# Performance work log

Measured on AMD Instinct MI355X. Metric: run time of the kernel, lower is better.

The kernel has to match this reference:

```python
import jax, jax.numpy as jnp
import numpy as np

B, N, D, H = 8, 2048, 768, 12
HD = D // H
SCALE = HD ** -0.5


def setup_inputs() -> dict:
    key = jax.random.key(0)
    ks = jax.random.split(key, 5)
    std = D ** -0.5
    return {
        "x": jax.random.normal(ks[0], (B, N, D), jnp.float32),
        "W_qkv": jax.random.normal(ks[1], (D, 3 * D), jnp.float32) * std,
        "b_qkv": jax.random.normal(ks[2], (3 * D,), jnp.float32) * 0.02,
        "W_out": jax.random.normal(ks[3], (D, D), jnp.float32) * std,
        "b_out": jax.random.normal(ks[4], (D,), jnp.float32) * 0.02,
    }


def reference(x, W_qkv, b_qkv, W_out, b_out):
    qkv = x @ W_qkv + b_qkv
    qkv = qkv.reshape(B, N, 3, H, HD).transpose(2, 0, 3, 1, 4)
    q, k, v = qkv[0], qkv[1], qkv[2]
    # scaled dot-product attention (dropout is identity in eval)
    attn = jnp.einsum("bhqd,bhkd->bhqk", q, k) * SCALE
    attn = jax.nn.softmax(attn, axis=-1)
    out = jnp.einsum("bhqk,bhkd->bhqd", attn, v)
    out = out.transpose(0, 2, 1, 3).reshape(B, N, D)
    return out @ W_out + b_out
```

## Files before the change

### kernel.cpp

```cpp
#include <hip/hip_runtime.h>
#include <hip/hip_bf16.h>
#include <stdint.h>

#define BB 8
#define NN 2048
#define DD 768
#define HH 12
#define HD 64
#define ND3 2304
#define TOK (BB*NN)
#define QSC 0.18033688011112042f

typedef __bf16 bf16x8 __attribute__((ext_vector_type(8)));
typedef float  f32x4  __attribute__((ext_vector_type(4)));
typedef float  f32x16 __attribute__((ext_vector_type(16)));
typedef unsigned uint2v __attribute__((ext_vector_type(2)));

__device__ __forceinline__ unsigned short f2bf(float f) {
    union { float f; unsigned u; } v; v.f = f;
    unsigned r = v.u + 0x7FFF + ((v.u >> 16) & 1);
    return (unsigned short)(r >> 16);
}
__device__ __forceinline__ unsigned packbf(float lo, float hi) {
    return __builtin_amdgcn_perm(__float_as_uint(hi) + 0x8000u,
                                 __float_as_uint(lo) + 0x8000u, 0x07060302u);
}
__device__ __forceinline__ unsigned cvtpk(float lo, float hi) {
    unsigned r;
    asm("v_cvt_pk_bf16_f32 %0, %1, %2" : "=v"(r) : "v"(lo), "v"(hi));
    return r;
}

__device__ __forceinline__ void gload_lds16(const unsigned short* g, unsigned short* l) {
    __builtin_amdgcn_global_load_lds((const __attribute__((address_space(1))) void*)g,
                                     (__attribute__((address_space(3))) void*)l, 16, 0, 0);
}

__global__ __launch_bounds__(256) void f32_to_bf16_vec(const float* __restrict__ in,
                                                       unsigned short* __restrict__ out, int n4) {
    int i = blockIdx.x * 256 + threadIdx.x;
    if (i < n4) {
        float4 v = reinterpret_cast<const float4*>(in)[i];
        ushort4 o;
        o.x = f2bf(v.x); o.y = f2bf(v.y); o.z = f2bf(v.z); o.w = f2bf(v.w);
        reinterpret_cast<ushort4*>(out)[i] = o;
    }
}

__global__ __launch_bounds__(256) void transpose_bf16(const float* __restrict__ in,
                                                      unsigned short* __restrict__ out,
                                                      int R, int C) {
    int idx = blockIdx.x * 256 + threadIdx.x;
    if (idx < R * C) {
        int ci = idx / R;
        int r  = idx - ci * R;
        out[(size_t)ci * R + r] = f2bf(in[(size_t)r * C + ci]);
    }
}

__global__ __launch_bounds__(256) void qkv_gemm(const unsigned short* __restrict__ xb,
                                                const unsigned short* __restrict__ wt,
                                                const float* __restrict__ bias,
                                                unsigned short* __restrict__ qb,
                                                unsigned short* __restrict__ kb,
                                                unsigned short* __restrict__ vt) {
    __shared__ __align__(16) unsigned short As[128 * 64];
    __shared__ __align__(16) unsigned short Bs[128 * 64];
    const int tid  = threadIdx.x;
    const int wave = tid >> 6;
    const int lane = tid & 63;
    const int qd   = lane >> 4;
    const int c    = lane & 15;
    const int m0 = blockIdx.y * 128;
    const int n0 = blockIdx.x * 128;
    const int wm = (wave >> 1) * 64;
    const int wn = (wave & 1) * 64;
    const int srow = lane >> 3;
    const int sch  = (lane & 7) ^ srow;

    const unsigned short* Ag = xb + (size_t)(m0 + wave * 32 + srow) * DD + sch * 8;
    const unsigned short* Bg = wt + (size_t)(n0 + wave * 32 + srow) * DD + sch * 8;
    const int csw = c & 7;

    f32x4 acc[4][4] = {};
    for (int k0 = 0; k0 < DD; k0 += 64) {
        #pragma unroll
        for (int j = 0; j < 4; ++j) {
            gload_lds16(Ag + (size_t)(j * 8) * DD + k0, &As[(wave * 32 + j * 8) * 64]);
            gload_lds16(Bg + (size_t)(j * 8) * DD + k0, &Bs[(wave * 32 + j * 8) * 64]);
        }
        __syncthreads();
        #pragma unroll
        for (int kk = 0; kk < 2; ++kk) {
            const int ch = (kk * 4 + qd) ^ csw;
            bf16x8 a[4], b[4];
            #pragma unroll
            for (int i = 0; i < 4; ++i)
                a[i] = *reinterpret_cast<const bf16x8*>(&As[(wm + i * 16 + c) * 64 + ch * 8]);
            #pragma unroll
            for (int j = 0; j < 4; ++j)
                b[j] = *reinterpret_cast<const bf16x8*>(&Bs[(wn + j * 16 + c) * 64 + ch * 8]);
            #pragma unroll
            for (int i = 0; i < 4; ++i)
                #pragma unroll
                for (int j = 0; j < 4; ++j)
                    acc[i][j] = __builtin_amdgcn_mfma_f32_16x16x32_bf16(a[i], b[j], acc[i][j], 0, 0, 0);
        }
        __syncthreads();
    }

    #pragma unroll
    for (int i = 0; i < 4; ++i)
        #pragma unroll
        for (int j = 0; j < 4; ++j)
            #pragma unroll
            for (int r = 0; r < 4; ++r) {
                int row = m0 + wm + i * 16 + qd * 4 + r;
                int col = n0 + wn + j * 16 + c;
                float v = acc[i][j][r] + bias[col];
                int t  = col / DD;
                int cc = col - t * DD;
                int hh = cc >> 6;
                int d  = cc & 63;
                int bi = row >> 11;
                int n  = row & (NN - 1);
                size_t bhh = (size_t)(bi * HH + hh);
                if (t == 0)      qb[(bhh * NN + n) * HD + d] = f2bf(v * QSC);
                else if (t == 1) kb[(bhh * NN + n) * HD + d] = f2bf(v);
                else             vt[(bhh * HD + d) * NN + n] = f2bf(v);
            }
}

__global__ __launch_bounds__(256) void attn_kernel(const unsigned short* __restrict__ qb,
                                                   const unsigned short* __restrict__ kb,
                                                   const unsigned short* __restrict__ vt,
                                                   unsigned short* __restrict__ ao) {
    __shared__ __align__(16) unsigned short Ks[2][64 * HD];
    __shared__ __align__(16) unsigned short Vs[2][64 * HD];

    const int blk  = blockIdx.x;
    const int xcd  = blk & 7;
    const int g    = blk >> 3;
    const int bh   = xcd * 12 + (g >> 4);
    const int qt   = g & 15;
    const int tid  = threadIdx.x;
    const int wave = tid >> 6;
    const int lane = tid & 63;
    const int col  = lane & 31;
    const int hf   = lane >> 5;
    const int q0   = qt * 128 + wave * 32;

    const unsigned short* Qp = qb + (size_t)bh * NN * HD;
    const unsigned short* Kp = kb + (size_t)bh * NN * HD;
    const unsigned short* Vp = vt + (size_t)bh * HD * NN;

    const int srow = lane >> 3;
    const int sch  = (lane & 7) ^ srow;

    bf16x8 aq[4];
    #pragma unroll
    for (int ks = 0; ks < 4; ++ks)
        aq[ks] = *reinterpret_cast<const bf16x8*>(Qp + (size_t)(q0 + col) * HD + ks * 16 + hf * 8);

    f32x16 ot[2] = {};
    f32x16 lacc  = {};
    const f32x16 zf = {};

    union { unsigned short u[8]; bf16x8 v; } onesb;
    #pragma unroll
    for (int i = 0; i < 8; ++i) onesb.u[i] = 0x3F80;

    #pragma unroll
    for (int j = 0; j < 2; ++j) {
        const int rb = wave * 16 + j * 8;
        gload_lds16(Kp + (size_t)(rb + srow) * HD + sch * 8, &Ks[0][rb * HD]);
        gload_lds16(Vp + (size_t)(rb + srow) * NN + sch * 8, &Vs[0][rb * HD]);
    }
    __syncthreads();

    #pragma unroll 1
    for (int kt = 0; kt < NN; kt += 64) {
        const int cur = (kt >> 6) & 1;

        if (kt + 64 < NN) {
            const int nb = cur ^ 1;
            #pragma unroll
            for (int j = 0; j < 2; ++j) {
                const int rb = wave * 16 + j * 8;
                gload_lds16(Kp + (size_t)(kt + 64 + rb + srow) * HD + sch * 8, &Ks[nb][rb * HD]);
                gload_lds16(Vp + (size_t)(rb + srow) * NN + kt + 64 + sch * 8, &Vs[nb][rb * HD]);
            }
        }

        const unsigned short* Ksb = &Ks[cur][0];
        const unsigned short* Vsb = &Vs[cur][0];
        const int cswz = col & 7;

        bf16x8 kf[8];
        #pragma unroll
        for (int nt = 0; nt < 2; ++nt)
            #pragma unroll
            for (int ks = 0; ks < 4; ++ks) {
                const int kr = nt * 32 + col;
                const int ch = ((ks << 1) + hf) ^ cswz;
                kf[nt * 4 + ks] = *reinterpret_cast<const bf16x8*>(Ksb + kr * HD + ch * 8);
            }

        f32x16 s[2];
        __builtin_amdgcn_s_setprio(1);
        #pragma unroll
        for (int nt = 0; nt < 2; ++nt) {
            s[nt] = __builtin_amdgcn_mfma_f32_32x32x16_bf16(kf[nt * 4 + 0], aq[0], zf, 0, 0, 0);
            #pragma unroll
            for (int ks = 1; ks < 4; ++ks)
                s[nt] = __builtin_amdgcn_mfma_f32_32x32x16_bf16(kf[nt * 4 + ks], aq[ks], s[nt], 0, 0, 0);
        }
        __builtin_amdgcn_s_setprio(0);

        unsigned pd[2][8];
        #pragma unroll
        for (int nt = 0; nt < 2; ++nt)
            #pragma unroll
            for (int gi = 0; gi < 8; ++gi) {
                float p0 = __builtin_amdgcn_exp2f(s[nt][2 * gi]);
                float p1 = __builtin_amdgcn_exp2f(s[nt][2 * gi + 1]);
                pd[nt][gi] = cvtpk(p0, p1);
            }

        #pragma unroll
        for (int kk = 0; kk < 4; ++kk) {
            const int nt = kk >> 1;
            const int bs = (kk & 1) * 4;
            const int ch = ((kk << 1) + hf) ^ cswz;
            bf16x8 v0 = *reinterpret_cast<const bf16x8*>(Vsb + col * HD + ch * 8);
            bf16x8 v1 = *reinterpret_cast<const bf16x8*>(Vsb + (32 + col) * HD + ch * 8);
            uint2v r02 = __builtin_amdgcn_permlane32_swap(pd[nt][bs + 0], pd[nt][bs + 2], false, false);
            uint2v r13 = __builtin_amdgcn_permlane32_swap(pd[nt][bs + 1], pd[nt][bs + 3], false, false);
            union { unsigned d[4]; bf16x8 v; } bfr;
            bfr.d[0] = r02.x;
            bfr.d[1] = r13.x;
            bfr.d[2] = r02.y;
            bfr.d[3] = r13.y;
            __builtin_amdgcn_s_setprio(1);
            ot[0] = __builtin_amdgcn_mfma_f32_32x32x16_bf16(v0, bfr.v, ot[0], 0, 0, 0);
            ot[1] = __builtin_amdgcn_mfma_f32_32x32x16_bf16(v1, bfr.v, ot[1], 0, 0, 0);
            lacc  = __builtin_amdgcn_mfma_f32_32x32x16_bf16(onesb.v, bfr.v, lacc, 0, 0, 0);
            __builtin_amdgcn_s_setprio(0);
        }

        __syncthreads();
    }

    float linv = 1.0f / lacc[0];
    const int bi = bh / HH;
    const int hh = bh - bi * HH;
    const int n  = q0 + col;
    size_t base = ((size_t)bi * NN + n) * DD + hh * HD;
    #pragma unroll
    for (int dt = 0; dt < 2; ++dt)
        #pragma unroll
        for (int g4 = 0; g4 < 4; ++g4) {
            uint2 dd2;
            dd2.x = packbf(ot[dt][4 * g4 + 0] * linv, ot[dt][4 * g4 + 1] * linv);
            dd2.y = packbf(ot[dt][4 * g4 + 2] * linv, ot[dt][4 * g4 + 3] * linv);
            *reinterpret_cast<uint2*>(&((unsigned short*)ao)[base + dt * 32 + g4 * 8 + hf * 4]) = dd2;
        }
}

__global__ __launch_bounds__(256) void out_gemm(const unsigned short* __restrict__ ab,
                                                const unsigned short* __restrict__ wt,
                                                const float* __restrict__ bias,
                                                float* __restrict__ out) {
    __shared__ __align__(16) unsigned short As[128 * 64];
    __shared__ __align__(16) unsigned short Bs[128 * 64];
    const int tid  = threadIdx.x;
    const int wave = tid >> 6;
    const int lane = tid & 63;
    const int qd   = lane >> 4;
    const int c    = lane & 15;
    const int m0 = blockIdx.y * 128;
    const int n0 = blockIdx.x * 128;
    const int wm = (wave >> 1) * 64;
    const int wn = (wave & 1) * 64;
    const int srow = lane >> 3;
    const int sch  = (lane & 7) ^ srow;

    const unsigned short* Ag = ab + (size_t)(m0 + wave * 32 + srow) * DD + sch * 8;
    const unsigned short* Bg = wt + (size_t)(n0 + wave * 32 + srow) * DD + sch * 8;
    const int csw = c & 7;

    f32x4 acc[4][4] = {};
    for (int k0 = 0; k0 < DD; k0 += 64) {
        #pragma unroll
        for (int j = 0; j < 4; ++j) {
            gload_lds16(Ag + (size_t)(j * 8) * DD + k0, &As[(wave * 32 + j * 8) * 64]);
            gload_lds16(Bg + (size_t)(j * 8) * DD + k0, &Bs[(wave * 32 + j * 8) * 64]);
        }
        __syncthreads();
        #pragma unroll
        for (int kk = 0; kk < 2; ++kk) {
            const int ch = (kk * 4 + qd) ^ csw;
            bf16x8 a[4], b[4];
            #pragma unroll
            for (int i = 0; i < 4; ++i)
                a[i] = *reinterpret_cast<const bf16x8*>(&As[(wm + i * 16 + c) * 64 + ch * 8]);
            #pragma unroll
            for (int j = 0; j < 4; ++j)
                b[j] = *reinterpret_cast<const bf16x8*>(&Bs[(wn + j * 16 + c) * 64 + ch * 8]);
            #pragma unroll
            for (int i = 0; i < 4; ++i)
                #pragma unroll
                for (int j = 0; j < 4; ++j)
                    acc[i][j] = __builtin_amdgcn_mfma_f32_16x16x32_bf16(a[i], b[j], acc[i][j], 0, 0, 0);
        }
        __syncthreads();
    }

    #pragma unroll
    for (int i = 0; i < 4; ++i)
        #pragma unroll
        for (int j = 0; j < 4; ++j)
            #pragma unroll
            for (int r = 0; r < 4; ++r) {
                int row = m0 + wm + i * 16 + qd * 4 + r;
                int col = n0 + wn + j * 16 + c;
                out[(size_t)row * DD + col] = acc[i][j][r] + bias[col];
            }
}

extern "C" void kernel_launch(void* const* d_in, const int* in_sizes, int n_in,
                              void* d_out, int out_size, void* d_ws, size_t ws_size,
                              hipStream_t stream) {
    const float* x     = (const float*)d_in[0];
    const float* W_qkv = (const float*)d_in[1];
    const float* b_qkv = (const float*)d_in[2];
    const float* W_out = (const float*)d_in[3];
    const float* b_out = (const float*)d_in[4];
    float* out = (float*)d_out;

    char* ws = (char*)d_ws;
    const size_t SZ_X   = (size_t)TOK * DD * 2;
    const size_t SZ_WQ  = (size_t)ND3 * DD * 2;
    const size_t SZ_WO  = (size_t)DD * DD * 2;
    const size_t SZ_QKV = (size_t)TOK * DD * 2;
    unsigned short* xb  = (unsigned short*)(ws);
    unsigned short* wtq = (unsigned short*)(ws + SZ_X);
    unsigned short* wto = (unsigned short*)(ws + SZ_X + SZ_WQ);
    unsigned short* qb  = (unsigned short*)(ws + SZ_X + SZ_WQ + SZ_WO);
    unsigned short* kb  = (unsigned short*)(ws + SZ_X + SZ_WQ + SZ_WO + SZ_QKV);
    unsigned short* vtb = (unsigned short*)(ws + SZ_X + SZ_WQ + SZ_WO + 2 * SZ_QKV);
    unsigned short* ao  = (unsigned short*)(ws + SZ_X + SZ_WQ + SZ_WO + 3 * SZ_QKV);

    {
        int n4 = TOK * DD / 4;
        f32_to_bf16_vec<<<(n4 + 255) / 256, 256, 0, stream>>>(x, xb, n4);
        int nq = DD * ND3;
        transpose_bf16<<<(nq + 255) / 256, 256, 0, stream>>>(W_qkv, wtq, DD, ND3);
        int no = DD * DD;
        transpose_bf16<<<(no + 255) / 256, 256, 0, stream>>>(W_out, wto, DD, DD);
    }
    qkv_gemm<<<dim3(ND3 / 128, TOK / 128), 256, 0, stream>>>(xb, wtq, b_qkv, qb, kb, vtb);
    attn_kernel<<<1536, 256, 0, stream>>>(qb, kb, vtb, ao);
    out_gemm<<<dim3(DD / 128, TOK / 128), 256, 0, stream>>>(ao, wto, b_out, out);
}
```

Measured before the change: 411.4 us.

## Double-buffer GEMM K-loop, swizzle workgroups, and tile weight transposes

Both projection GEMMs now use a double-buffered LDS pipeline with a K-step of 32, so the global-to-LDS load for the next tile is issued before the MFMAs on the current one. This costs one barrier per step instead of two. Workgroup IDs are remapped in groups of 8 for better L2 locality, and s_setprio raises wave priority around the MFMA block. The naive strided weight transpose is replaced by a 32x32 LDS-tiled transpose so reads and writes are coalesced. The XOR swizzle on LDS reads is dropped, which may cause bank conflicts, and the smaller K-step doubles the number of loop iterations.

```diff
diff --git a/kernel.cpp b/kernel.cpp
--- a/kernel.cpp
+++ b/kernel.cpp
@@ -47,15 +47,22 @@
     }
 }
 
-__global__ __launch_bounds__(256) void transpose_bf16(const float* __restrict__ in,
-                                                      unsigned short* __restrict__ out,
-                                                      int R, int C) {
-    int idx = blockIdx.x * 256 + threadIdx.x;
-    if (idx < R * C) {
-        int ci = idx / R;
-        int r  = idx - ci * R;
-        out[(size_t)ci * R + r] = f2bf(in[(size_t)r * C + ci]);
-    }
+__global__ __launch_bounds__(256) void transpose_bf16_tiled(const float* __restrict__ in,
+                                                            unsigned short* __restrict__ out,
+                                                            int R, int C) {
+    __shared__ float t[32][33];
+    const int tid = threadIdx.x;
+    const int tc = tid & 31;
+    const int tr = tid >> 5;
+    const int r0 = blockIdx.y * 32;
+    const int c0 = blockIdx.x * 32;
+    #pragma unroll
+    for (int j = 0; j < 4; ++j)
+        t[tr + j * 8][tc] = in[(size_t)(r0 + tr + j * 8) * C + c0 + tc];
+    __syncthreads();
+    #pragma unroll
+    for (int j = 0; j < 4; ++j)
+        out[(size_t)(c0 + tr + j * 8) * R + r0 + tc] = f2bf(t[tc][tr + j * 8]);
 }
 
 __global__ __launch_bounds__(256) void qkv_gemm(const unsigned short* __restrict__ xb,
@@ -64,48 +71,61 @@
                                                 unsigned short* __restrict__ qb,
                                                 unsigned short* __restrict__ kb,
                                                 unsigned short* __restrict__ vt) {
-    __shared__ __align__(16) unsigned short As[128 * 64];
-    __shared__ __align__(16) unsigned short Bs[128 * 64];
+    __shared__ __align__(16) unsigned short As[2][128 * 32];
+    __shared__ __align__(16) unsigned short Bs[2][128 * 32];
     const int tid  = threadIdx.x;
     const int wave = tid >> 6;
     const int lane = tid & 63;
     const int qd   = lane >> 4;
     const int c    = lane & 15;
-    const int m0 = blockIdx.y * 128;
-    const int n0 = blockIdx.x * 128;
+
+    const int nbx  = gridDim.x;
+    const int nwg  = nbx * gridDim.y;
+    const int orig = blockIdx.y * nbx + blockIdx.x;
+    const int swz  = (orig & 7) * (nwg >> 3) + (orig >> 3);
+    const int m0 = (swz / nbx) * 128;
+    const int n0 = (swz % nbx) * 128;
+
     const int wm = (wave >> 1) * 64;
     const int wn = (wave & 1) * 64;
-    const int srow = lane >> 3;
-    const int sch  = (lane & 7) ^ srow;
-
-    const unsigned short* Ag = xb + (size_t)(m0 + wave * 32 + srow) * DD + sch * 8;
-    const unsigned short* Bg = wt + (size_t)(n0 + wave * 32 + srow) * DD + sch * 8;
-    const int csw = c & 7;
+
+    const unsigned short* Ag = xb + (size_t)(m0 + wave * 32 + (lane >> 2)) * DD + (lane & 3) * 8;
+    const unsigned short* Bg = wt + (size_t)(n0 + wave * 32 + (lane >> 2)) * DD + (lane & 3) * 8;
+    const int rb = wave * 32;
+
+    #pragma unroll
+    for (int j = 0; j < 2; ++j) {
+        gload_lds16(Ag + (size_t)(j * 16) * DD, &As[0][(rb + j * 16) * 32]);
+        gload_lds16(Bg + (size_t)(j * 16) * DD, &Bs[0][(rb + j * 16) * 32]);
+    }
+    __syncthreads();
 
     f32x4 acc[4][4] = {};
-    for (int k0 = 0; k0 < DD; k0 += 64) {
-        #pragma unroll
-        for (int j = 0; j < 4; ++j) {
-            gload_lds16(Ag + (size_t)(j * 8) * DD + k0, &As[(wave * 32 + j * 8) * 64]);
-            gload_lds16(Bg + (size_t)(j * 8) * DD + k0, &Bs[(wave * 32 + j * 8) * 64]);
-        }
-        __syncthreads();
-        #pragma unroll
-        for (int kk = 0; kk < 2; ++kk) {
-            const int ch = (kk * 4 + qd) ^ csw;
-            bf16x8 a[4], b[4];
-            #pragma unroll
-            for (int i = 0; i < 4; ++i)
-                a[i] = *reinterpret_cast<const bf16x8*>(&As[(wm + i * 16 + c) * 64 + ch * 8]);
+    #pragma unroll 1
+    for (int t = 0; t < DD / 32; ++t) {
+        const int cur = t & 1;
+        if (t + 1 < DD / 32) {
+            const int k1 = (t + 1) * 32;
+            #pragma unroll
+            for (int j = 0; j < 2; ++j) {
+                gload_lds16(Ag + (size_t)(j * 16) * DD + k1, &As[cur ^ 1][(rb + j * 16) * 32]);
+                gload_lds16(Bg + (size_t)(j * 16) * DD + k1, &Bs[cur ^ 1][(rb + j * 16) * 32]);
+            }
+        }
+        bf16x8 a[4], b[4];
+        #pragma unroll
+        for (int i = 0; i < 4; ++i)
+            a[i] = *reinterpret_cast<const bf16x8*>(&As[cur][(wm + i * 16 + c) * 32 + qd * 8]);
+        #pragma unroll
+        for (int j = 0; j < 4; ++j)
+            b[j] = *reinterpret_cast<const bf16x8*>(&Bs[cur][(wn + j * 16 + c) * 32 + qd * 8]);
+        __builtin_amdgcn_s_setprio(1);
+        #pragma unroll
+        for (int i = 0; i < 4; ++i)
             #pragma unroll
             for (int j = 0; j < 4; ++j)
-                b[j] = *reinterpret_cast<const bf16x8*>(&Bs[(wn + j * 16 + c) * 64 + ch * 8]);
-            #pragma unroll
-            for (int i = 0; i < 4; ++i)
-                #pragma unroll
-                for (int j = 0; j < 4; ++j)
-                    acc[i][j] = __builtin_amdgcn_mfma_f32_16x16x32_bf16(a[i], b[j], acc[i][j], 0, 0, 0);
-        }
+                acc[i][j] = __builtin_amdgcn_mfma_f32_16x16x32_bf16(a[i], b[j], acc[i][j], 0, 0, 0);
+        __builtin_amdgcn_s_setprio(0);
         __syncthreads();
     }
 
@@ -271,48 +291,61 @@
                                                 const unsigned short* __restrict__ wt,
                                                 const float* __restrict__ bias,
                                                 float* __restrict__ out) {
-    __shared__ __align__(16) unsigned short As[128 * 64];
-    __shared__ __align__(16) unsigned short Bs[128 * 64];
+    __shared__ __align__(16) unsigned short As[2][128 * 32];
+    __shared__ __align__(16) unsigned short Bs[2][128 * 32];
     const int tid  = threadIdx.x;
     const int wave = tid >> 6;
     const int lane = tid & 63;
     const int qd   = lane >> 4;
     const int c    = lane & 15;
-    const int m0 = blockIdx.y * 128;
-    const int n0 = blockIdx.x * 128;
+
+    const int nbx  = gridDim.x;
+    const int nwg  = nbx * gridDim.y;
+    const int orig = blockIdx.y * nbx + blockIdx.x;
+    const int swz  = (orig & 7) * (nwg >> 3) + (orig >> 3);
+    const int m0 = (swz / nbx) * 128;
+    const int n0 = (swz % nbx) * 128;
+
     const int wm = (wave >> 1) * 64;
     const int wn = (wave & 1) * 64;
-    const int srow = lane >> 3;
-    const int sch  = (lane & 7) ^ srow;
-
-    const unsigned short* Ag = ab + (size_t)(m0 + wave * 32 + srow) * DD + sch * 8;
-    const unsigned short* Bg = wt + (size_t)(n0 + wave * 32 + srow) * DD + sch * 8;
-    const int csw = c & 7;
+
+    const unsigned short* Ag = ab + (size_t)(m0 + wave * 32 + (lane >> 2)) * DD + (lane & 3) * 8;
+    const unsigned short* Bg = wt + (size_t)(n0 + wave * 32 + (lane >> 2)) * DD + (lane & 3) * 8;
+    const int rb = wave * 32;
+
+    #pragma unroll
+    for (int j = 0; j < 2; ++j) {
+        gload_lds16(Ag + (size_t)(j * 16) * DD, &As[0][(rb + j * 16) * 32]);
+        gload_lds16(Bg + (size_t)(j * 16) * DD, &Bs[0][(rb + j * 16) * 32]);
+    }
+    __syncthreads();
 
     f32x4 acc[4][4] = {};
-    for (int k0 = 0; k0 < DD; k0 += 64) {
-        #pragma unroll
-        for (int j = 0; j < 4; ++j) {
-            gload_lds16(Ag + (size_t)(j * 8) * DD + k0, &As[(wave * 32 + j * 8) * 64]);
-            gload_lds16(Bg + (size_t)(j * 8) * DD + k0, &Bs[(wave * 32 + j * 8) * 64]);
-        }
-        __syncthreads();
-        #pragma unroll
-        for (int kk = 0; kk < 2; ++kk) {
-            const int ch = (kk * 4 + qd) ^ csw;
-            bf16x8 a[4], b[4];
-            #pragma unroll
-            for (int i = 0; i < 4; ++i)
-                a[i] = *reinterpret_cast<const bf16x8*>(&As[(wm + i * 16 + c) * 64 + ch * 8]);
+    #pragma unroll 1
+    for (int t = 0; t < DD / 32; ++t) {
+        const int cur = t & 1;
+        if (t + 1 < DD / 32) {
+            const int k1 = (t + 1) * 32;
+            #pragma unroll
+            for (int j = 0; j < 2; ++j) {
+                gload_lds16(Ag + (size_t)(j * 16) * DD + k1, &As[cur ^ 1][(rb + j * 16) * 32]);
+                gload_lds16(Bg + (size_t)(j * 16) * DD + k1, &Bs[cur ^ 1][(rb + j * 16) * 32]);
+            }
+        }
+        bf16x8 a[4], b[4];
+        #pragma unroll
+        for (int i = 0; i < 4; ++i)
+            a[i] = *reinterpret_cast<const bf16x8*>(&As[cur][(wm + i * 16 + c) * 32 + qd * 8]);
+        #pragma unroll
+        for (int j = 0; j < 4; ++j)
+            b[j] = *reinterpret_cast<const bf16x8*>(&Bs[cur][(wn + j * 16 + c) * 32 + qd * 8]);
+        __builtin_amdgcn_s_setprio(1);
+        #pragma unroll
+        for (int i = 0; i < 4; ++i)
             #pragma unroll
             for (int j = 0; j < 4; ++j)
-                b[j] = *reinterpret_cast<const bf16x8*>(&Bs[(wn + j * 16 + c) * 64 + ch * 8]);
-            #pragma unroll
-            for (int i = 0; i < 4; ++i)
-                #pragma unroll
-                for (int j = 0; j < 4; ++j)
-                    acc[i][j] = __builtin_amdgcn_mfma_f32_16x16x32_bf16(a[i], b[j], acc[i][j], 0, 0, 0);
-        }
+                acc[i][j] = __builtin_amdgcn_mfma_f32_16x16x32_bf16(a[i], b[j], acc[i][j], 0, 0, 0);
+        __builtin_amdgcn_s_setprio(0);
         __syncthreads();
     }
 
@@ -354,10 +387,8 @@
     {
         int n4 = TOK * DD / 4;
         f32_to_bf16_vec<<<(n4 + 255) / 256, 256, 0, stream>>>(x, xb, n4);
-        int nq = DD * ND3;
-        transpose_bf16<<<(nq + 255) / 256, 256, 0, stream>>>(W_qkv, wtq, DD, ND3);
-        int no = DD * DD;
-        transpose_bf16<<<(no + 255) / 256, 256, 0, stream>>>(W_out, wto, DD, DD);
+        transpose_bf16_tiled<<<dim3(ND3 / 32, DD / 32), 256, 0, stream>>>(W_qkv, wtq, DD, ND3);
+        transpose_bf16_tiled<<<dim3(DD / 32, DD / 32), 256, 0, stream>>>(W_out, wto, DD, DD);
     }
     qkv_gemm<<<dim3(ND3 / 128, TOK / 128), 256, 0, stream>>>(xb, wtq, b_qkv, qb, kb, vtb);
     attn_kernel<<<1536, 256, 0, stream>>>(qb, kb, vtb, ao);
```

After: 393.7 us. 4.3% less time.
